# Performance work log

Hardware: AMD Instinct MI355X
Metric: run time of the kernel (lower is better)

The kernel has to match this reference:

```python
import jax, jax.numpy as jnp
import numpy as np

H = 12  # num_heads (init kwarg)


def setup_inputs() -> dict:
    key = jax.random.key(0)
    ks = jax.random.split(key, 9)
    B, S, D, M = 2, 1025, 768, 4
    hw = S - 1
    x = jax.random.normal(ks[0], (B, S, D), dtype=jnp.float32)
    masks = jax.random.randint(ks[1], (B, M, hw), 0, 2, dtype=jnp.int32)
    init = lambda k: jax.random.normal(k, (D, D), dtype=jnp.float32) * 0.02
    return {
        'x': x, 'masks': masks,
        'Wq': init(ks[2]), 'bq': jnp.zeros((D,), jnp.float32),
        'Wk': init(ks[3]), 'bk': jnp.zeros((D,), jnp.float32),
        'Wv': init(ks[4]), 'bv': jnp.zeros((D,), jnp.float32),
    }


def reference(x, masks, Wq, bq, Wk, bk, Wv, bv):
    B, S, D = x.shape
    hd = D // H
    scale = 1.0 / jnp.sqrt(jnp.asarray(hd, x.dtype))

    def heads(t):  # (B,S,D) -> (B,H,S,hd)
        return t.reshape(B, S, H, hd).transpose(0, 2, 1, 3)

    q = heads(x @ Wq.T + bq)
    k = heads(x @ Wk.T + bk)
    v = heads(x @ Wv.T + bv)

    scores_ori = jnp.einsum('bhqd,bhkd->bhqk', q, k) * scale  # (B,H,S,S)
    attn = jax.nn.softmax(scores_ori, axis=-1)  # dropout is identity at eval
    h = jnp.einsum('bhqk,bhkd->bhqd', attn, v)
    h = h.transpose(0, 2, 1, 3).reshape(B, S, D)

    # ---- mask-expanded attention (torch.no_grad branch) ----
    Mk, hw = masks.shape[1], masks.shape[2]
    m = masks.astype(x.dtype)  # (B,M,hw)
    # pad: position 0 (CLS) gets 0, positions 1..hw get the mask
    new_masks = jnp.pad(m, ((0, 0), (0, 0), (1, S - 1 - hw)))  # (B,M,S)
    bias = -10000.0 * (1.0 - new_masks)  # additive mask bias
    new_scores = scores_ori[:, None] + bias[:, :, None, None, :]  # (B,M,H,S,S)
    new_attn = jax.nn.softmax(new_scores, axis=-1)
    new_h = jnp.einsum('bmhqk,bhkd->bmhqd', new_attn, v)  # v repeated per mask
    new_h = new_h.transpose(0, 1, 3, 2, 4).reshape(B * Mk, S, D)

    img_idx = jnp.repeat(jnp.arange(B), Mk)  # [0]*M + [1]*M + ...
    new_x = jnp.broadcast_to(x[:, None], (B, Mk, S, D)).reshape(B * Mk, S, D)
    return (h, new_h, img_idx, new_x)
```

## Files before the change

kernel.cpp:

```cpp
#include <hip/hip_runtime.h>

typedef float f32x4 __attribute__((ext_vector_type(4)));
typedef short s16x8 __attribute__((ext_vector_type(8)));

constexpr int B  = 2;
constexpr int S  = 1025;
constexpr int D  = 768;
constexpr int DD = D * D;
constexpr int H  = 12;
constexpr int NM = 4;
constexpr int ROWS = B * S;
constexpr int BSD  = B * S * D;
constexpr int SP   = 1088;
constexpr int OUT_NEWH_OFF = BSD;
constexpr int OUT_IDX_OFF  = BSD + NM * BSD;
constexpr int OUT_NEWX_OFF = OUT_IDX_OFF + B * NM;

__device__ __forceinline__ unsigned short f2bf(float f) {
    unsigned u = __builtin_bit_cast(unsigned, f);
    u += 0x7FFF + ((u >> 16) & 1);
    return (unsigned short)(u >> 16);
}

__device__ __forceinline__ void gll16(const void* g, void* l) {
    __builtin_amdgcn_global_load_lds(
        (const __attribute__((address_space(1))) void*)g,
        (__attribute__((address_space(3))) void*)l, 16, 0, 0);
}

__global__ __launch_bounds__(256) void conv_kernel(
    const float* __restrict__ x, const float* __restrict__ Wq,
    const float* __restrict__ Wk, const float* __restrict__ Wv,
    unsigned short* __restrict__ xb, unsigned short* __restrict__ Wb,
    unsigned short* __restrict__ Vt)
{
    constexpr int NX8 = BSD / 8;
    constexpr int NW8 = DD / 8;
    constexpr int TOT = NX8 + 3 * NW8;
    const int tid = blockIdx.x * 256 + threadIdx.x;
    for (int c = tid; c < TOT; c += gridDim.x * 256) {
        const float* src;
        unsigned short* dst;
        if (c < NX8) { src = x + (size_t)c * 8; dst = xb + (size_t)c * 8; }
        else {
            const int cc = c - NX8;
            const int mt = cc / NW8;
            const int rr = cc - mt * NW8;
            src = ((mt == 0) ? Wq : (mt == 1) ? Wk : Wv) + (size_t)rr * 8;
            dst = Wb + (size_t)mt * DD + (size_t)rr * 8;
        }
        const float4 a = *(const float4*)src;
        const float4 b2 = *(const float4*)(src + 4);
        s16x8 v;
        v[0] = (short)f2bf(a.x);  v[1] = (short)f2bf(a.y);
        v[2] = (short)f2bf(a.z);  v[3] = (short)f2bf(a.w);
        v[4] = (short)f2bf(b2.x); v[5] = (short)f2bf(b2.y);
        v[6] = (short)f2bf(b2.z); v[7] = (short)f2bf(b2.w);
        *(s16x8*)dst = v;
    }
    constexpr int NPADC = SP - S;
    constexpr int NPAD = B * H * 64 * NPADC;
    if (tid < NPAD) {
        const int row = tid / NPADC;
        const int s = S + (tid % NPADC);
        Vt[(size_t)row * SP + s] = 0;
    }
}

__global__ __launch_bounds__(256, 2) void qkv_mfma_kernel(
    const unsigned short* __restrict__ xb, const unsigned short* __restrict__ Wb,
    const float* __restrict__ bq, const float* __restrict__ bk,
    const float* __restrict__ bv,
    unsigned short* __restrict__ Qb, unsigned short* __restrict__ Kb,
    unsigned short* __restrict__ Vt)
{
    __shared__ __align__(16) unsigned short Xs[2][64 * 64];
    __shared__ __align__(16) unsigned short Wl[2][64 * 64];

    const int t = threadIdx.x;
    const int row0 = blockIdx.x * 64;
    const int yy = blockIdx.y;
    const int mt = yy / 12;
    const int col0 = (yy % 12) * 64;
    const float* bias = (mt == 0) ? bq : (mt == 1) ? bk : bv;
    const unsigned short* Wsrc = Wb + (size_t)mt * DD;

    const int w = t >> 6, l = t & 63, lq = l & 15, grp = l >> 4;

    auto stage = [&](int buf, int k0) {
        #pragma unroll
        for (int i = 0; i < 2; ++i) {
            const int slot = i * 256 + t;
            const int r = slot >> 3, cl = slot & 7;
            const int cg = cl ^ (r & 7);
            int row = row0 + r; if (row > ROWS - 1) row = ROWS - 1;
            gll16(xb + (size_t)row * D + k0 + cg * 8, &Xs[buf][slot * 8]);
            gll16(Wsrc + (size_t)(col0 + r) * D + k0 + cg * 8, &Wl[buf][slot * 8]);
        }
    };

    f32x4 acc[4] = {};
    stage(0, 0);

    for (int ks = 0; ks < 12; ++ks) {
        const int cur = ks & 1;
        __syncthreads();
        if (ks + 1 < 12) stage(cur ^ 1, (ks + 1) * 64);

        s16x8 a[2];
        const int xr = w * 16 + lq;
        #pragma unroll
        for (int kh = 0; kh < 2; ++kh)
            a[kh] = *(const s16x8*)&Xs[cur][xr * 64 + (((kh * 4 + grp) ^ (xr & 7)) * 8)];
        #pragma unroll
        for (int nt = 0; nt < 4; ++nt) {
            const int wr = nt * 16 + lq;
            #pragma unroll
            for (int kh = 0; kh < 2; ++kh) {
                s16x8 bfr = *(const s16x8*)&Wl[cur][wr * 64 + (((kh * 4 + grp) ^ (wr & 7)) * 8)];
                acc[nt] = __builtin_amdgcn_mfma_f32_16x16x32_bf16(a[kh], bfr, acc[nt], 0, 0, 0);
            }
        }
    }

    #pragma unroll
    for (int nt = 0; nt < 4; ++nt) {
        const int col = col0 + nt * 16 + lq;
        const float bv_ = bias[col];
        #pragma unroll
        for (int r = 0; r < 4; ++r) {
            const int row = row0 + w * 16 + grp * 4 + r;
            if (row >= ROWS) continue;
            const unsigned short val = f2bf(acc[nt][r] + bv_);
            if (mt == 0)      Qb[(size_t)row * D + col] = val;
            else if (mt == 1) Kb[(size_t)row * D + col] = val;
            else {
                const int bb = (row >= S) ? 1 : 0;
                const int s  = row - bb * S;
                const int hh = col >> 6, dd = col & 63;
                Vt[((size_t)((bb * H + hh) * 64 + dd)) * SP + s] = val;
            }
        }
    }
}

__global__ __launch_bounds__(128, 2) void attn_mfma_kernel(
    const unsigned short* __restrict__ Qb, const unsigned short* __restrict__ Kb,
    const unsigned short* __restrict__ Vt, const int* __restrict__ masks,
    float* __restrict__ out_h, float* __restrict__ out_newh)
{
    __shared__ __align__(16) unsigned short Kl[2][64 * 64];
    __shared__ __align__(16) unsigned short Vl[2][64 * 64];
    __shared__ __align__(16) unsigned short Pl[2][16 * 64];
    __shared__ __align__(16) float          Mf[2][4][64];
    __shared__ __align__(16) unsigned short Mm[2][4 * 64];

    const int t = threadIdx.x;
    const int qt = blockIdx.x, hh = blockIdx.y, b = blockIdx.z;
    const int q0 = qt * 32;
    const int w = t >> 6, l = t & 63, lq = l & 15, grp = l >> 4;

    s16x8 qf[2] = {};
    {
        const int row = q0 + w * 16 + lq;
        if (row < S) {
            const unsigned short* p = Qb + (size_t)(b * S + row) * D + hh * 64 + grp * 8;
            qf[0] = *(const s16x8*)(p);
            qf[1] = *(const s16x8*)(p + 32);
        }
    }

    const unsigned short* Kbase = Kb + (size_t)b * S * D + hh * 64;
    const unsigned short* Vbase = Vt + (size_t)(b * H + hh) * 64 * SP;

    auto stage = [&](int buf, int it) {
        const int k0 = it * 64;
        #pragma unroll
        for (int i = 0; i < 4; ++i) {
            const int slot = i * 128 + t;
            const int r = slot >> 3, cl = slot & 7;
            const int cg = cl ^ (r & 7);
            int p = k0 + r; if (p > S - 1) p = S - 1;
            gll16(Kbase + (size_t)p * D + cg * 8, &Kl[buf][slot * 8]);
        }
        #pragma unroll
        for (int i = 0; i < 4; ++i) {
            const int slot = i * 128 + t;
            const int r = slot >> 3, cl = slot & 7;
            const int cg = cl ^ (r & 7);
            gll16(Vbase + (size_t)r * SP + k0 + cg * 8, &Vl[buf][slot * 8]);
        }
        #pragma unroll
        for (int j = 0; j < 2; ++j) {
            const int idx = j * 128 + t;
            const int v = idx >> 6, kk = idx & 63;
            const int p = k0 + kk;
            const int m = (p >= 1 && p < S) ? masks[(size_t)(b * NM + v) * (S - 1) + p - 1] : 0;
            Mf[buf][v][kk] = (float)m;
            Mm[buf][v * 64 + kk] = m ? 0xFFFFu : 0u;
        }
    };

    f32x4 acc[5][4] = {};
    float sums[5][4] = {};

    stage(0, 0);

    constexpr int NT = 17;
    for (int it = 0; it < NT; ++it) {
        const int cur = it & 1;
        __syncthreads();
        if (it + 1 < NT) stage(cur ^ 1, it + 1);
        const int k0 = it * 64;

        f32x4 qk[4] = {};
        #pragma unroll
        for (int kt = 0; kt < 4; ++kt) {
            const int kr = kt * 16 + lq;
            #pragma unroll
            for (int kh = 0; kh < 2; ++kh) {
                s16x8 kf = *(const s16x8*)&Kl[cur][kr * 64 + (((kh * 4 + grp) ^ (kr & 7)) * 8)];
                qk[kt] = __builtin_amdgcn_mfma_f32_16x16x32_bf16(qf[kh], kf, qk[kt], 0, 0, 0);
            }
        }

        #pragma unroll
        for (int kt = 0; kt < 4; ++kt) {
            const int kloc = kt * 16 + lq;
            const int kg = k0 + kloc;
            const float mf0 = Mf[cur][0][kloc], mf1 = Mf[cur][1][kloc];
            const float mf2 = Mf[cur][2][kloc], mf3 = Mf[cur][3][kloc];
            #pragma unroll
            for (int r = 0; r < 4; ++r) {
                const float e = (kg < S) ? __expf(qk[kt][r] * 0.125f) : 0.f;
                sums[0][r] += e;
                sums[1][r] += mf0 * e; sums[2][r] += mf1 * e;
                sums[3][r] += mf2 * e; sums[4][r] += mf3 * e;
                const int q = grp * 4 + r;
                Pl[w][q * 64 + (((kloc >> 3) ^ (q & 7)) * 8) + (kloc & 7)] = f2bf(e);
            }
        }

        #pragma unroll
        for (int h2 = 0; h2 < 2; ++h2) {
            s16x8 ea = *(const s16x8*)&Pl[w][lq * 64 + (((h2 * 4 + grp) ^ (lq & 7)) * 8)];
            s16x8 pa[5];
            pa[0] = ea;
            #pragma unroll
            for (int v = 1; v < 5; ++v) {
                s16x8 mm = *(const s16x8*)&Mm[cur][(v - 1) * 64 + (h2 * 4 + grp) * 8];
                pa[v] = ea & mm;
            }
            #pragma unroll
            for (int dt = 0; dt < 4; ++dt) {
                const int dr = dt * 16 + lq;
                s16x8 vb = *(const s16x8*)&Vl[cur][dr * 64 + (((h2 * 4 + grp) ^ (dr & 7)) * 8)];
                #pragma unroll
                for (int v = 0; v < 5; ++v)
                    acc[v][dt] = __builtin_amdgcn_mfma_f32_16x16x32_bf16(pa[v], vb, acc[v][dt], 0, 0, 0);
            }
        }
    }

    #pragma unroll
    for (int m = 1; m < 16; m <<= 1)
        #pragma unroll
        for (int v = 0; v < 5; ++v)
            #pragma unroll
            for (int r = 0; r < 4; ++r)
                sums[v][r] += __shfl_xor(sums[v][r], m);

    #pragma unroll
    for (int r = 0; r < 4; ++r) {
        const int q = q0 + w * 16 + grp * 4 + r;
        if (q >= S) continue;
        #pragma unroll
        for (int v = 0; v < 5; ++v) {
            const float inv = 1.0f / sums[v][r];
            float* outp = (v == 0)
                ? out_h    + (size_t)(b * S + q) * D + hh * 64 + lq
                : out_newh + (size_t)((b * NM + v - 1) * S + q) * D + hh * 64 + lq;
            #pragma unroll
            for (int dt = 0; dt < 4; ++dt)
                outp[dt * 16] = acc[v][dt][r] * inv;
        }
    }
}

__global__ __launch_bounds__(256) void tail_kernel(
    const float* __restrict__ x, float* __restrict__ out_newx,
    float* __restrict__ out_idx)
{
    const int SLAB4  = S * D / 4;
    const int TOTAL4 = B * NM * SLAB4;
    const float4* x4 = (const float4*)x;
    float4* o4 = (float4*)out_newx;
    for (int f = blockIdx.x * blockDim.x + threadIdx.x; f < TOTAL4;
         f += gridDim.x * blockDim.x) {
        const int bm  = f / SLAB4;
        const int rem = f - bm * SLAB4;
        o4[f] = x4[(bm >> 2) * SLAB4 + rem];
    }
    const int idx = blockIdx.x * blockDim.x + threadIdx.x;
    if (idx < B * NM) out_idx[idx] = (float)(idx >> 2);
}

extern "C" void kernel_launch(void* const* d_in, const int* in_sizes, int n_in,
                              void* d_out, int out_size, void* d_ws, size_t ws_size,
                              hipStream_t stream)
{
    const float* x     = (const float*)d_in[0];
    const int*   masks = (const int*)  d_in[1];
    const float* Wq    = (const float*)d_in[2];
    const float* bq    = (const float*)d_in[3];
    const float* Wk    = (const float*)d_in[4];
    const float* bk    = (const float*)d_in[5];
    const float* Wv    = (const float*)d_in[6];
    const float* bv    = (const float*)d_in[7];

    float* out = (float*)d_out;
    float* out_h    = out;
    float* out_newh = out + OUT_NEWH_OFF;
    float* out_idx  = out + OUT_IDX_OFF;
    float* out_newx = out + OUT_NEWX_OFF;

    unsigned short* Qb = (unsigned short*)d_ws;
    unsigned short* Kb = Qb + BSD;
    unsigned short* Vt = Kb + BSD;

    unsigned short* xb = (unsigned short*)out_newx;
    unsigned short* Wb = xb + BSD;

    conv_kernel<<<1634, 256, 0, stream>>>(x, Wq, Wk, Wv, xb, Wb, Vt);
    {
        dim3 grid(33, 36);
        qkv_mfma_kernel<<<grid, 256, 0, stream>>>(xb, Wb, bq, bk, bv, Qb, Kb, Vt);
    }
    {
        dim3 grid(33, H, B);
        attn_mfma_kernel<<<grid, 128, 0, stream>>>(Qb, Kb, Vt, masks,
                                                   out_h, out_newh);
    }
    tail_kernel<<<2048, 256, 0, stream>>>(x, out_newx, out_idx);
}
```

Before: 99.97 us.

## Restructure attention into single-wave blocks with register-resident K/V and MFMA row sums

Rewrites the attention kernel so each 64-thread block handles 16 queries. K and V fragments are loaded straight from global memory into registers with software prefetch, replacing the LDS staging and block barriers. The softmax scale is folded into Q during the projection epilogue. Row sums come from an extra MFMA against a ones vector instead of per-lane accumulation and shuffles. Mask bitmasks are precomputed once in the conversion kernel, and blocks are remapped for XCD locality. This trades more global/L2 traffic for K/V reuse (each block re-reads K/V for only 16 queries) against less LDS and sync overhead.

Result: slower. 139.0 us (+39.1%).

```diff
diff --git a/kernel.cpp b/kernel.cpp
--- a/kernel.cpp
+++ b/kernel.cpp
@@ -12,9 +12,12 @@
 constexpr int ROWS = B * S;
 constexpr int BSD  = B * S * D;
 constexpr int SP   = 1088;
+constexpr int KPAD = 1088;
 constexpr int OUT_NEWH_OFF = BSD;
 constexpr int OUT_IDX_OFF  = BSD + NM * BSD;
 constexpr int OUT_NEWX_OFF = OUT_IDX_OFF + B * NM;
+
+#define QSCALE 0.125f
 
 __device__ __forceinline__ unsigned short f2bf(float f) {
     unsigned u = __builtin_bit_cast(unsigned, f);
@@ -31,8 +34,9 @@
 __global__ __launch_bounds__(256) void conv_kernel(
     const float* __restrict__ x, const float* __restrict__ Wq,
     const float* __restrict__ Wk, const float* __restrict__ Wv,
+    const int* __restrict__ masks,
     unsigned short* __restrict__ xb, unsigned short* __restrict__ Wb,
-    unsigned short* __restrict__ Vt)
+    unsigned short* __restrict__ Vt, unsigned short* __restrict__ Mmb)
 {
     constexpr int NX8 = BSD / 8;
     constexpr int NW8 = DD / 8;
@@ -65,6 +69,12 @@
         const int s = S + (tid % NPADC);
         Vt[(size_t)row * SP + s] = 0;
     }
+    if (tid < B * NM * KPAD) {
+        const int k  = tid % KPAD;
+        const int bv = tid / KPAD;
+        const int m = (k >= 1 && k < S) ? masks[(size_t)bv * (S - 1) + k - 1] : 0;
+        Mmb[tid] = m ? 0xFFFFu : 0u;
+    }
 }
 
 __global__ __launch_bounds__(256, 2) void qkv_mfma_kernel(
@@ -131,158 +141,146 @@
         for (int r = 0; r < 4; ++r) {
             const int row = row0 + w * 16 + grp * 4 + r;
             if (row >= ROWS) continue;
-            const unsigned short val = f2bf(acc[nt][r] + bv_);
-            if (mt == 0)      Qb[(size_t)row * D + col] = val;
-            else if (mt == 1) Kb[(size_t)row * D + col] = val;
+            const float raw = acc[nt][r] + bv_;
+            if (mt == 0)      Qb[(size_t)row * D + col] = f2bf(raw * QSCALE);
+            else if (mt == 1) Kb[(size_t)row * D + col] = f2bf(raw);
             else {
                 const int bb = (row >= S) ? 1 : 0;
                 const int s  = row - bb * S;
                 const int hh = col >> 6, dd = col & 63;
-                Vt[((size_t)((bb * H + hh) * 64 + dd)) * SP + s] = val;
+                Vt[((size_t)((bb * H + hh) * 64 + dd)) * SP + s] = f2bf(raw);
             }
         }
     }
 }
 
-__global__ __launch_bounds__(128, 2) void attn_mfma_kernel(
+__global__ __launch_bounds__(64) void attn_mfma_kernel(
     const unsigned short* __restrict__ Qb, const unsigned short* __restrict__ Kb,
-    const unsigned short* __restrict__ Vt, const int* __restrict__ masks,
+    const unsigned short* __restrict__ Vt, const unsigned short* __restrict__ Mmb,
     float* __restrict__ out_h, float* __restrict__ out_newh)
 {
-    __shared__ __align__(16) unsigned short Kl[2][64 * 64];
-    __shared__ __align__(16) unsigned short Vl[2][64 * 64];
     __shared__ __align__(16) unsigned short Pl[2][16 * 64];
-    __shared__ __align__(16) float          Mf[2][4][64];
-    __shared__ __align__(16) unsigned short Mm[2][4 * 64];
-
-    const int t = threadIdx.x;
-    const int qt = blockIdx.x, hh = blockIdx.y, b = blockIdx.z;
-    const int q0 = qt * 32;
-    const int w = t >> 6, l = t & 63, lq = l & 15, grp = l >> 4;
+
+    const int orig = blockIdx.x;
+    const int wgid = (orig & 7) * 195 + (orig >> 3);
+    const int hb = wgid / 65;
+    const int qt = wgid - hb * 65;
+    const int b  = hb / H, hh = hb - b * H;
+    const int q0 = qt * 16;
+
+    const int l = threadIdx.x;
+    const int lq = l & 15, grp = l >> 4;
+
+    const unsigned short* Kbase = Kb + (size_t)(b * S) * D + hh * 64 + grp * 8;
+    const unsigned short* Vbase = Vt + (size_t)hb * 64 * SP + grp * 8;
+    const unsigned short* Mbase = Mmb + (size_t)b * NM * KPAD + grp * 8;
 
     s16x8 qf[2] = {};
-    {
-        const int row = q0 + w * 16 + lq;
-        if (row < S) {
-            const unsigned short* p = Qb + (size_t)(b * S + row) * D + hh * 64 + grp * 8;
-            qf[0] = *(const s16x8*)(p);
-            qf[1] = *(const s16x8*)(p + 32);
-        }
-    }
-
-    const unsigned short* Kbase = Kb + (size_t)b * S * D + hh * 64;
-    const unsigned short* Vbase = Vt + (size_t)(b * H + hh) * 64 * SP;
-
-    auto stage = [&](int buf, int it) {
-        const int k0 = it * 64;
-        #pragma unroll
-        for (int i = 0; i < 4; ++i) {
-            const int slot = i * 128 + t;
-            const int r = slot >> 3, cl = slot & 7;
-            const int cg = cl ^ (r & 7);
-            int p = k0 + r; if (p > S - 1) p = S - 1;
-            gll16(Kbase + (size_t)p * D + cg * 8, &Kl[buf][slot * 8]);
-        }
-        #pragma unroll
-        for (int i = 0; i < 4; ++i) {
-            const int slot = i * 128 + t;
-            const int r = slot >> 3, cl = slot & 7;
-            const int cg = cl ^ (r & 7);
-            gll16(Vbase + (size_t)r * SP + k0 + cg * 8, &Vl[buf][slot * 8]);
-        }
-        #pragma unroll
-        for (int j = 0; j < 2; ++j) {
-            const int idx = j * 128 + t;
-            const int v = idx >> 6, kk = idx & 63;
-            const int p = k0 + kk;
-            const int m = (p >= 1 && p < S) ? masks[(size_t)(b * NM + v) * (S - 1) + p - 1] : 0;
-            Mf[buf][v][kk] = (float)m;
-            Mm[buf][v * 64 + kk] = m ? 0xFFFFu : 0u;
+    if (q0 + lq < S) {
+        const unsigned short* p = Qb + (size_t)(b * S + q0 + lq) * D + hh * 64 + grp * 8;
+        qf[0] = *(const s16x8*)p;
+        qf[1] = *(const s16x8*)(p + 32);
+    }
+
+    s16x8 onesf;
+    #pragma unroll
+    for (int i = 0; i < 8; ++i) onesf[i] = (short)0x3F80;
+
+    s16x8 kf[4][2];
+    s16x8 vf[4][2];
+
+    auto load_k = [&](int k0) {
+        #pragma unroll
+        for (int kt = 0; kt < 4; ++kt) {
+            int row = k0 + kt * 16 + lq; if (row > S - 1) row = S - 1;
+            const unsigned short* p = Kbase + (size_t)row * D;
+            kf[kt][0] = *(const s16x8*)p;
+            kf[kt][1] = *(const s16x8*)(p + 32);
         }
     };
-
-    f32x4 acc[5][4] = {};
-    float sums[5][4] = {};
-
-    stage(0, 0);
+    auto load_v = [&](int k0) {
+        #pragma unroll
+        for (int dt = 0; dt < 4; ++dt) {
+            const unsigned short* p = Vbase + (size_t)(dt * 16 + lq) * SP + k0;
+            vf[dt][0] = *(const s16x8*)p;
+            vf[dt][1] = *(const s16x8*)(p + 32);
+        }
+    };
+
+    f32x4 acc[5][5] = {};
+
+    load_k(0);
+    load_v(0);
 
     constexpr int NT = 17;
     for (int it = 0; it < NT; ++it) {
-        const int cur = it & 1;
-        __syncthreads();
-        if (it + 1 < NT) stage(cur ^ 1, it + 1);
         const int k0 = it * 64;
+        unsigned short* P = &Pl[it & 1][0];
 
         f32x4 qk[4] = {};
         #pragma unroll
+        for (int kt = 0; kt < 4; ++kt)
+            #pragma unroll
+            for (int kh = 0; kh < 2; ++kh)
+                qk[kt] = __builtin_amdgcn_mfma_f32_16x16x32_bf16(kf[kt][kh], qf[kh], qk[kt], 0, 0, 0);
+
+        if (it + 1 < NT) load_k(k0 + 64);
+
+        #pragma unroll
         for (int kt = 0; kt < 4; ++kt) {
-            const int kr = kt * 16 + lq;
-            #pragma unroll
-            for (int kh = 0; kh < 2; ++kh) {
-                s16x8 kf = *(const s16x8*)&Kl[cur][kr * 64 + (((kh * 4 + grp) ^ (kr & 7)) * 8)];
-                qk[kt] = __builtin_amdgcn_mfma_f32_16x16x32_bf16(qf[kh], kf, qk[kt], 0, 0, 0);
+            float e[4];
+            #pragma unroll
+            for (int r = 0; r < 4; ++r) {
+                const int key = k0 + kt * 16 + grp * 4 + r;
+                e[r] = (key < S) ? __expf(qk[kt][r]) : 0.f;
             }
-        }
-
-        #pragma unroll
-        for (int kt = 0; kt < 4; ++kt) {
-            const int kloc = kt * 16 + lq;
-            const int kg = k0 + kloc;
-            const float mf0 = Mf[cur][0][kloc], mf1 = Mf[cur][1][kloc];
-            const float mf2 = Mf[cur][2][kloc], mf3 = Mf[cur][3][kloc];
-            #pragma unroll
-            for (int r = 0; r < 4; ++r) {
-                const float e = (kg < S) ? __expf(qk[kt][r] * 0.125f) : 0.f;
-                sums[0][r] += e;
-                sums[1][r] += mf0 * e; sums[2][r] += mf1 * e;
-                sums[3][r] += mf2 * e; sums[4][r] += mf3 * e;
-                const int q = grp * 4 + r;
-                Pl[w][q * 64 + (((kloc >> 3) ^ (q & 7)) * 8) + (kloc & 7)] = f2bf(e);
-            }
-        }
-
-        #pragma unroll
-        for (int h2 = 0; h2 < 2; ++h2) {
-            s16x8 ea = *(const s16x8*)&Pl[w][lq * 64 + (((h2 * 4 + grp) ^ (lq & 7)) * 8)];
+            const unsigned p01 = (unsigned)f2bf(e[0]) | ((unsigned)f2bf(e[1]) << 16);
+            const unsigned p23 = (unsigned)f2bf(e[2]) | ((unsigned)f2bf(e[3]) << 16);
+            const int chunk = kt * 2 + (grp >> 1);
+            *(uint2*)&P[lq * 64 + ((chunk ^ (lq & 7)) * 8) + (grp & 1) * 4] =
+                make_uint2(p01, p23);
+        }
+
+        #pragma unroll
+        for (int kh = 0; kh < 2; ++kh) {
+            s16x8 mm[4];
+            #pragma unroll
+            for (int v = 0; v < 4; ++v)
+                mm[v] = *(const s16x8*)(Mbase + (size_t)v * KPAD + k0 + kh * 32);
+
             s16x8 pa[5];
-            pa[0] = ea;
-            #pragma unroll
-            for (int v = 1; v < 5; ++v) {
-                s16x8 mm = *(const s16x8*)&Mm[cur][(v - 1) * 64 + (h2 * 4 + grp) * 8];
-                pa[v] = ea & mm;
-            }
-            #pragma unroll
-            for (int dt = 0; dt < 4; ++dt) {
-                const int dr = dt * 16 + lq;
-                s16x8 vb = *(const s16x8*)&Vl[cur][dr * 64 + (((h2 * 4 + grp) ^ (dr & 7)) * 8)];
+            pa[0] = *(const s16x8*)&P[lq * 64 + (((kh * 4 + grp) ^ (lq & 7)) * 8)];
+            #pragma unroll
+            for (int v = 1; v < 5; ++v) pa[v] = pa[0] & mm[v - 1];
+
+            #pragma unroll
+            for (int dt = 0; dt < 4; ++dt)
                 #pragma unroll
                 for (int v = 0; v < 5; ++v)
-                    acc[v][dt] = __builtin_amdgcn_mfma_f32_16x16x32_bf16(pa[v], vb, acc[v][dt], 0, 0, 0);
+                    acc[v][dt] = __builtin_amdgcn_mfma_f32_16x16x32_bf16(vf[dt][kh], pa[v], acc[v][dt], 0, 0, 0);
+            #pragma unroll
+            for (int v = 0; v < 5; ++v)
+                acc[v][4] = __builtin_amdgcn_mfma_f32_16x16x32_bf16(onesf, pa[v], acc[v][4], 0, 0, 0);
+        }
+
+        if (it + 1 < NT) load_v(k0 + 64);
+    }
+
+    const int q = q0 + lq;
+    if (q < S) {
+        #pragma unroll
+        for (int v = 0; v < 5; ++v) {
+            const float inv = 1.0f / acc[v][4][0];
+            float* base = ((v == 0)
+                ? out_h    + (size_t)(b * S + q) * D
+                : out_newh + (size_t)((b * NM + v - 1) * S + q) * D) + hh * 64 + grp * 4;
+            #pragma unroll
+            for (int dt = 0; dt < 4; ++dt) {
+                float4 o;
+                o.x = acc[v][dt][0] * inv; o.y = acc[v][dt][1] * inv;
+                o.z = acc[v][dt][2] * inv; o.w = acc[v][dt][3] * inv;
+                *(float4*)(base + dt * 16) = o;
             }
-        }
-    }
-
-    #pragma unroll
-    for (int m = 1; m < 16; m <<= 1)
-        #pragma unroll
-        for (int v = 0; v < 5; ++v)
-            #pragma unroll
-            for (int r = 0; r < 4; ++r)
-                sums[v][r] += __shfl_xor(sums[v][r], m);
-
-    #pragma unroll
-    for (int r = 0; r < 4; ++r) {
-        const int q = q0 + w * 16 + grp * 4 + r;
-        if (q >= S) continue;
-        #pragma unroll
-        for (int v = 0; v < 5; ++v) {
-            const float inv = 1.0f / sums[v][r];
-            float* outp = (v == 0)
-                ? out_h    + (size_t)(b * S + q) * D + hh * 64 + lq
-                : out_newh + (size_t)((b * NM + v - 1) * S + q) * D + hh * 64 + lq;
-            #pragma unroll
-            for (int dt = 0; dt < 4; ++dt)
-                outp[dt * 16] = acc[v][dt][r] * inv;
         }
     }
 }
@@ -324,22 +322,19 @@
     float* out_idx  = out + OUT_IDX_OFF;
     float* out_newx = out + OUT_NEWX_OFF;
 
-    unsigned short* Qb = (unsigned short*)d_ws;
-    unsigned short* Kb = Qb + BSD;
-    unsigned short* Vt = Kb + BSD;
+    unsigned short* Qb  = (unsigned short*)d_ws;
+    unsigned short* Kb  = Qb + BSD;
+    unsigned short* Vt  = Kb + BSD;
+    unsigned short* Mmb = Vt + (size_t)B * H * 64 * SP;
 
     unsigned short* xb = (unsigned short*)out_newx;
     unsigned short* Wb = xb + BSD;
 
-    conv_kernel<<<1634, 256, 0, stream>>>(x, Wq, Wk, Wv, xb, Wb, Vt);
+    conv_kernel<<<1634, 256, 0, stream>>>(x, Wq, Wk, Wv, masks, xb, Wb, Vt, Mmb);
     {
         dim3 grid(33, 36);
         qkv_mfma_kernel<<<grid, 256, 0, stream>>>(xb, Wb, bq, bk, bv, Qb, Kb, Vt);
     }
-    {
-        dim3 grid(33, H, B);
-        attn_mfma_kernel<<<grid, 128, 0, stream>>>(Qb, Kb, Vt, masks,
-                                                   out_h, out_newh);
-    }
+    attn_mfma_kernel<<<1560, 64, 0, stream>>>(Qb, Kb, Vt, Mmb, out_h, out_newh);
     tail_kernel<<<2048, 256, 0, stream>>>(x, out_newx, out_idx);
 }
```
